# Kernel tuning notes

Measured on AMD Instinct MI355X. Metric: run time of the kernel, lower is better.

Reference implementation:

```python
import jax, jax.numpy as jnp
import numpy as np

N_NODES = 50000
N_EDGES = 800000
C_IN = 128
C_OUT = 128


def setup_inputs() -> dict:
    key = jax.random.key(0)
    k1, k2, k3 = jax.random.split(key, 3)
    x = jax.random.normal(k1, (N_NODES, C_IN), dtype=jnp.float32)
    edge_index = jax.random.randint(k2, (2, N_EDGES), 0, N_NODES, dtype=jnp.int64)
    # Glorot-style init for the GCN weight, zero bias (PyG defaults)
    scale = jnp.sqrt(2.0 / (C_IN + C_OUT)).astype(jnp.float32)
    weight = jax.random.normal(k3, (C_IN, C_OUT), dtype=jnp.float32) * scale
    bias = jnp.zeros((C_OUT,), dtype=jnp.float32)
    return {"x": x, "edge_index": edge_index, "weight": weight, "bias": bias}


def reference(x, edge_index, weight, bias):
    # GCNConv (edge_weight=None): out = D^-1/2 (A+I) D^-1/2 (x @ W) + b, then ReLU.
    # Dropout is identity in eval mode.
    n = x.shape[0]
    loops = jnp.arange(n, dtype=edge_index.dtype)
    src = jnp.concatenate([edge_index[0], loops])  # [E+N] message sources j
    dst = jnp.concatenate([edge_index[1], loops])  # [E+N] aggregation targets i
    ew = jnp.ones(src.shape[0], dtype=x.dtype)
    # degree computed at target nodes (PyG gcn_norm uses col)
    deg = jax.ops.segment_sum(ew, dst, num_segments=n)
    deg_inv_sqrt = jnp.where(deg > 0, jax.lax.rsqrt(jnp.maximum(deg, 1.0)), 0.0)
    norm = deg_inv_sqrt[src] * deg_inv_sqrt[dst]  # [E+N]
    h = x @ weight                                 # [N, C_out]
    msg = h[src] * norm[:, None]                   # gather + scale  [E+N, C_out]
    agg = jax.ops.segment_sum(msg, dst, num_segments=n)  # scatter-add SpMM
    return jax.nn.relu(agg + bias)
```

## Files before the change

### kernel.cpp

```cpp
#include <hip/hip_runtime.h>
#include <cstdint>
#include <cstddef>

#define NCH 128
#define GEMM_ROWS 64
#define XPAD 136
#define CAP 64

typedef short bf16x8 __attribute__((ext_vector_type(8)));
typedef float f32x4 __attribute__((ext_vector_type(4)));
typedef int i32x4 __attribute__((ext_vector_type(4)));

__device__ __forceinline__ int detect_is64(const unsigned int* __restrict__ ei) {
  unsigned int v = ei[((threadIdx.x & 63) << 1) + 1];
  return (__ballot(v != 0u) == 0ULL) ? 1 : 0;
}

__device__ __forceinline__ unsigned short f2bf(float x) {
  unsigned int u = __float_as_uint(x);
  u += 0x7fffu + ((u >> 16) & 1u);
  return (unsigned short)(u >> 16);
}

__device__ __forceinline__ int ei_at(const void* ei, long long i, int is64) {
  return is64 ? (int)((const long long*)ei)[i] : ((const int*)ei)[i];
}

__global__ __launch_bounds__(256) void k_gemm_fill(
    const float* __restrict__ x, const float* __restrict__ W,
    unsigned short* __restrict__ g, int N, const void* __restrict__ ei, int E,
    int* __restrict__ cnt, int* __restrict__ bucket, int gbl) {
  if ((int)blockIdx.x >= gbl) {
    int is64 = detect_is64((const unsigned int*)ei);
    int base = ((int)blockIdx.x - gbl) * 2048 + (int)threadIdx.x * 8;
    if (base >= E) return;
    if (base + 8 <= E) {
      int s[8], d[8];
      if (is64) {
        const long long* ps = (const long long*)ei + base;
        const long long* pd = (const long long*)ei + E + base;
#pragma unroll
        for (int j = 0; j < 8; ++j) { s[j] = (int)ps[j]; d[j] = (int)pd[j]; }
      } else {
        const int4* ps = (const int4*)((const int*)ei + base);
        const int4* pd = (const int4*)((const int*)ei + E + base);
        int4 a = ps[0], b = ps[1], c = pd[0], dd = pd[1];
        s[0] = a.x; s[1] = a.y; s[2] = a.z; s[3] = a.w;
        s[4] = b.x; s[5] = b.y; s[6] = b.z; s[7] = b.w;
        d[0] = c.x; d[1] = c.y; d[2] = c.z; d[3] = c.w;
        d[4] = dd.x; d[5] = dd.y; d[6] = dd.z; d[7] = dd.w;
      }
      int slot[8];
#pragma unroll
      for (int j = 0; j < 8; ++j) slot[j] = atomicAdd(&cnt[d[j]], 1);
#pragma unroll
      for (int j = 0; j < 8; ++j)
        if (slot[j] < CAP) bucket[(size_t)d[j] * CAP + slot[j]] = s[j];
    } else {
      for (int j = 0; j < 8; ++j)
        if (base + j < E) {
          int s = ei_at(ei, base + j, is64);
          int d = ei_at(ei, (long long)E + base + j, is64);
          int slot = atomicAdd(&cnt[d], 1);
          if (slot < CAP) bucket[(size_t)d * CAP + slot] = s;
        }
    }
    return;
  }
  __shared__ unsigned short xbf[GEMM_ROWS * XPAD];
  int t = threadIdx.x;
  int row0 = blockIdx.x * GEMM_ROWS;
#pragma unroll
  for (int j = 0; j < 8; ++j) {
    int idx = t + 256 * j;
    int r = idx >> 5, ch = idx & 31;
    int row = row0 + r;
    float4 v = (row < N) ? ((const float4*)(x + (size_t)row * NCH))[ch]
                         : make_float4(0.f, 0.f, 0.f, 0.f);
    ushort4 p;
    p.x = f2bf(v.x); p.y = f2bf(v.y); p.z = f2bf(v.z); p.w = f2bf(v.w);
    *(ushort4*)&xbf[r * XPAD + ch * 4] = p;
  }
  int lane = t & 63, wv = t >> 6;
  int n0 = wv * 32, l15 = lane & 15, q = lane >> 4;
  bf16x8 B[4][2];
#pragma unroll
  for (int ks = 0; ks < 4; ++ks)
#pragma unroll
    for (int nt = 0; nt < 2; ++nt) {
      int n = n0 + nt * 16 + l15;
      bf16x8 b;
#pragma unroll
      for (int j = 0; j < 8; ++j)
        b[j] = (short)f2bf(W[(size_t)(ks * 32 + q * 8 + j) * NCH + n]);
      B[ks][nt] = b;
    }
  __syncthreads();
  f32x4 acc[4][2];
#pragma unroll
  for (int mt = 0; mt < 4; ++mt)
#pragma unroll
    for (int nt = 0; nt < 2; ++nt)
#pragma unroll
      for (int i = 0; i < 4; ++i) acc[mt][nt][i] = 0.f;
#pragma unroll
  for (int ks = 0; ks < 4; ++ks) {
#pragma unroll
    for (int mt = 0; mt < 4; ++mt) {
      bf16x8 a = *(const bf16x8*)&xbf[(mt * 16 + l15) * XPAD + ks * 32 + q * 8];
      acc[mt][0] = __builtin_amdgcn_mfma_f32_16x16x32_bf16(a, B[ks][0], acc[mt][0], 0, 0, 0);
      acc[mt][1] = __builtin_amdgcn_mfma_f32_16x16x32_bf16(a, B[ks][1], acc[mt][1], 0, 0, 0);
    }
  }
#pragma unroll
  for (int mt = 0; mt < 4; ++mt) {
#pragma unroll
    for (int reg = 0; reg < 4; ++reg) {
      int rl = mt * 16 + q * 4 + reg;
      int row = row0 + rl;
      if (row < N) {
        size_t base = (size_t)row * NCH + n0;
        g[base + l15]      = f2bf(acc[mt][0][reg]);
        g[base + 16 + l15] = f2bf(acc[mt][1][reg]);
      }
    }
  }
}

__device__ __forceinline__ void acc8(float* a, uint4 v, float w) {
  a[0] = fmaf(__uint_as_float(v.x << 16), w, a[0]);
  a[1] = fmaf(__uint_as_float(v.x & 0xffff0000u), w, a[1]);
  a[2] = fmaf(__uint_as_float(v.y << 16), w, a[2]);
  a[3] = fmaf(__uint_as_float(v.y & 0xffff0000u), w, a[3]);
  a[4] = fmaf(__uint_as_float(v.z << 16), w, a[4]);
  a[5] = fmaf(__uint_as_float(v.z & 0xffff0000u), w, a[5]);
  a[6] = fmaf(__uint_as_float(v.w << 16), w, a[6]);
  a[7] = fmaf(__uint_as_float(v.w & 0xffff0000u), w, a[7]);
}

__global__ __launch_bounds__(256) void k_agg(const unsigned short* __restrict__ g,
                                             const int* __restrict__ cnt,
                                             const int* __restrict__ bucket,
                                             const float* __restrict__ bias,
                                             float* __restrict__ out, int N) {
  int i = blockIdx.x * 4 + (threadIdx.x >> 6);
  if (i >= N) return;
  int lane = threadIdx.x & 63;
  int grp = lane >> 4, sl = lane & 15;
  float a[8];
#pragma unroll
  for (int k = 0; k < 8; ++k) a[k] = 0.f;
  int mt = cnt[i];
  float di = rsqrtf((float)(mt + 1));
  int m = mt < CAP ? mt : CAP;
  if (grp == 0) {
    uint4 v = *(const uint4*)(g + (size_t)i * NCH + sl * 8);
    acc8(a, v, di);
  }
  const int* brow = bucket + (size_t)i * CAP;
  int e = 0;
  for (; e + 16 <= m; e += 16) {
    i32x4 sv = *(const i32x4*)(brow + e + 4 * grp);
    float w[4];
    uint4 v[4];
#pragma unroll
    for (int j = 0; j < 4; ++j) {
      v[j] = *(const uint4*)(g + (size_t)sv[j] * NCH + sl * 8);
      w[j] = rsqrtf((float)(cnt[sv[j]] + 1));
    }
#pragma unroll
    for (int j = 0; j < 4; ++j) acc8(a, v[j], w[j]);
  }
  for (; e < m; e += 4) {
    int idx = e + grp;
    int cl = idx < m ? idx : m - 1;
    int s = brow[cl];
    float w = (idx < m) ? rsqrtf((float)(cnt[s] + 1)) : 0.f;
    uint4 v = *(const uint4*)(g + (size_t)s * NCH + sl * 8);
    acc8(a, v, w);
  }
#pragma unroll
  for (int k = 0; k < 8; ++k) {
    a[k] += __shfl_xor(a[k], 16);
    a[k] += __shfl_xor(a[k], 32);
  }
  if (grp == 0) {
    const float4* bb = (const float4*)bias;
    float4 b0 = bb[sl * 2], b1 = bb[sl * 2 + 1];
    f32x4 o0, o1;
    o0[0] = fmaxf(fmaf(a[0], di, b0.x), 0.f);
    o0[1] = fmaxf(fmaf(a[1], di, b0.y), 0.f);
    o0[2] = fmaxf(fmaf(a[2], di, b0.z), 0.f);
    o0[3] = fmaxf(fmaf(a[3], di, b0.w), 0.f);
    o1[0] = fmaxf(fmaf(a[4], di, b1.x), 0.f);
    o1[1] = fmaxf(fmaf(a[5], di, b1.y), 0.f);
    o1[2] = fmaxf(fmaf(a[6], di, b1.z), 0.f);
    o1[3] = fmaxf(fmaf(a[7], di, b1.w), 0.f);
    float* op = out + (size_t)i * NCH + sl * 8;
    __builtin_nontemporal_store(o0, (f32x4*)op);
    __builtin_nontemporal_store(o1, (f32x4*)(op + 4));
  }
}

extern "C" void kernel_launch(void* const* d_in, const int* in_sizes, int n_in,
                              void* d_out, int out_size, void* d_ws, size_t ws_size,
                              hipStream_t stream) {
  const float* x    = (const float*)d_in[0];
  const void*  ei   = d_in[1];
  const float* W    = (const float*)d_in[2];
  const float* bias = (const float*)d_in[3];
  float* out = (float*)d_out;

  int N = out_size / NCH;
  int E = in_sizes[1] / 2;

  char* ws = (char*)d_ws;
  size_t off = 0;
  auto alloc = [&](size_t bytes) -> char* {
    char* p = ws + off;
    off = (off + bytes + 255) & ~(size_t)255;
    return p;
  };
  char* zbase = ws;
  int*            cnt    = (int*)alloc((size_t)N * 4);
  size_t zbytes = off;
  int*            bucket = (int*)alloc((size_t)N * CAP * 4);
  unsigned short* g      = (unsigned short*)alloc((size_t)N * NCH * 2);
  (void)ws_size;

  int gbl  = (N + GEMM_ROWS - 1) / GEMM_ROWS;
  int cbl8 = (E + 2047) / 2048;

  (void)hipMemsetAsync(zbase, 0, zbytes, stream);
  k_gemm_fill<<<gbl + cbl8, 256, 0, stream>>>(x, W, g, N, ei, E, cnt, bucket, gbl);
  k_agg<<<(N + 3) / 4, 256, 0, stream>>>(g, cnt, bucket, bias, out, N);
}
```

Before: 161.9 us.

## Reorder fill blocks first, shrink edges per thread, batch 8 gathers in aggregation

The fused kernel now places the edge-bucketing blocks before the GEMM blocks, so the atomic-heavy fill work is dispatched first. Each fill thread now handles 4 edges instead of 8, which doubles the number of fill blocks. In the aggregation kernel, each 16-lane group now loads 8 neighbor indices and issues 8 row gathers per iteration, covering 32 edges per pass with masked tails. This gives more gathers in flight and removes the separate remainder loop, at the cost of more registers and wasted masked loads for low-degree nodes.

```diff
diff --git a/kernel.cpp b/kernel.cpp
--- a/kernel.cpp
+++ b/kernel.cpp
@@ -9,7 +9,6 @@
 
 typedef short bf16x8 __attribute__((ext_vector_type(8)));
 typedef float f32x4 __attribute__((ext_vector_type(4)));
-typedef int i32x4 __attribute__((ext_vector_type(4)));
 
 __device__ __forceinline__ int detect_is64(const unsigned int* __restrict__ ei) {
   unsigned int v = ei[((threadIdx.x & 63) << 1) + 1];
@@ -26,38 +25,35 @@
   return is64 ? (int)((const long long*)ei)[i] : ((const int*)ei)[i];
 }
 
-__global__ __launch_bounds__(256) void k_gemm_fill(
+__global__ __launch_bounds__(256) void k_fill_gemm(
     const float* __restrict__ x, const float* __restrict__ W,
     unsigned short* __restrict__ g, int N, const void* __restrict__ ei, int E,
-    int* __restrict__ cnt, int* __restrict__ bucket, int gbl) {
-  if ((int)blockIdx.x >= gbl) {
+    int* __restrict__ cnt, int* __restrict__ bucket, int fbl) {
+  if ((int)blockIdx.x < fbl) {
     int is64 = detect_is64((const unsigned int*)ei);
-    int base = ((int)blockIdx.x - gbl) * 2048 + (int)threadIdx.x * 8;
+    int base = (int)blockIdx.x * 1024 + (int)threadIdx.x * 4;
     if (base >= E) return;
-    if (base + 8 <= E) {
-      int s[8], d[8];
+    if (base + 4 <= E) {
+      int s[4], d[4];
       if (is64) {
         const long long* ps = (const long long*)ei + base;
         const long long* pd = (const long long*)ei + E + base;
 #pragma unroll
-        for (int j = 0; j < 8; ++j) { s[j] = (int)ps[j]; d[j] = (int)pd[j]; }
+        for (int j = 0; j < 4; ++j) { s[j] = (int)ps[j]; d[j] = (int)pd[j]; }
       } else {
-        const int4* ps = (const int4*)((const int*)ei + base);
-        const int4* pd = (const int4*)((const int*)ei + E + base);
-        int4 a = ps[0], b = ps[1], c = pd[0], dd = pd[1];
+        int4 a = *(const int4*)((const int*)ei + base);
+        int4 c = *(const int4*)((const int*)ei + E + base);
         s[0] = a.x; s[1] = a.y; s[2] = a.z; s[3] = a.w;
-        s[4] = b.x; s[5] = b.y; s[6] = b.z; s[7] = b.w;
         d[0] = c.x; d[1] = c.y; d[2] = c.z; d[3] = c.w;
-        d[4] = dd.x; d[5] = dd.y; d[6] = dd.z; d[7] = dd.w;
       }
-      int slot[8];
-#pragma unroll
-      for (int j = 0; j < 8; ++j) slot[j] = atomicAdd(&cnt[d[j]], 1);
-#pragma unroll
-      for (int j = 0; j < 8; ++j)
+      int slot[4];
+#pragma unroll
+      for (int j = 0; j < 4; ++j) slot[j] = atomicAdd(&cnt[d[j]], 1);
+#pragma unroll
+      for (int j = 0; j < 4; ++j)
         if (slot[j] < CAP) bucket[(size_t)d[j] * CAP + slot[j]] = s[j];
     } else {
-      for (int j = 0; j < 8; ++j)
+      for (int j = 0; j < 4; ++j)
         if (base + j < E) {
           int s = ei_at(ei, base + j, is64);
           int d = ei_at(ei, (long long)E + base + j, is64);
@@ -69,7 +65,7 @@
   }
   __shared__ unsigned short xbf[GEMM_ROWS * XPAD];
   int t = threadIdx.x;
-  int row0 = blockIdx.x * GEMM_ROWS;
+  int row0 = ((int)blockIdx.x - fbl) * GEMM_ROWS;
 #pragma unroll
   for (int j = 0; j < 8; ++j) {
     int idx = t + 256 * j;
@@ -150,34 +146,32 @@
   float a[8];
 #pragma unroll
   for (int k = 0; k < 8; ++k) a[k] = 0.f;
-  int mt = cnt[i];
-  float di = rsqrtf((float)(mt + 1));
-  int m = mt < CAP ? mt : CAP;
+  int deg = cnt[i];
+  float di = rsqrtf((float)(deg + 1));
+  int m = deg < CAP ? deg : CAP;
   if (grp == 0) {
     uint4 v = *(const uint4*)(g + (size_t)i * NCH + sl * 8);
     acc8(a, v, di);
   }
   const int* brow = bucket + (size_t)i * CAP;
-  int e = 0;
-  for (; e + 16 <= m; e += 16) {
-    i32x4 sv = *(const i32x4*)(brow + e + 4 * grp);
-    float w[4];
-    uint4 v[4];
-#pragma unroll
-    for (int j = 0; j < 4; ++j) {
-      v[j] = *(const uint4*)(g + (size_t)sv[j] * NCH + sl * 8);
-      w[j] = rsqrtf((float)(cnt[sv[j]] + 1));
-    }
-#pragma unroll
-    for (int j = 0; j < 4; ++j) acc8(a, v[j], w[j]);
-  }
-  for (; e < m; e += 4) {
-    int idx = e + grp;
-    int cl = idx < m ? idx : m - 1;
-    int s = brow[cl];
-    float w = (idx < m) ? rsqrtf((float)(cnt[s] + 1)) : 0.f;
-    uint4 v = *(const uint4*)(g + (size_t)s * NCH + sl * 8);
-    acc8(a, v, w);
+  for (int e0 = 0; e0 < m; e0 += 32) {
+    int b = e0 + 8 * grp;
+    int s[8];
+    float w[8];
+#pragma unroll
+    for (int j = 0; j < 8; ++j) {
+      int idx = b + j;
+      int cl = idx < m ? idx : m - 1;
+      s[j] = brow[cl];
+    }
+    uint4 v[8];
+#pragma unroll
+    for (int j = 0; j < 8; ++j) {
+      v[j] = *(const uint4*)(g + (size_t)s[j] * NCH + sl * 8);
+      w[j] = (b + j < m) ? rsqrtf((float)(cnt[s[j]] + 1)) : 0.f;
+    }
+#pragma unroll
+    for (int j = 0; j < 8; ++j) acc8(a, v[j], w[j]);
   }
 #pragma unroll
   for (int k = 0; k < 8; ++k) {
@@ -228,10 +222,10 @@
   unsigned short* g      = (unsigned short*)alloc((size_t)N * NCH * 2);
   (void)ws_size;
 
-  int gbl  = (N + GEMM_ROWS - 1) / GEMM_ROWS;
-  int cbl8 = (E + 2047) / 2048;
+  int gbl = (N + GEMM_ROWS - 1) / GEMM_ROWS;
+  int fbl = (E + 1023) / 1024;
 
   (void)hipMemsetAsync(zbase, 0, zbytes, stream);
-  k_gemm_fill<<<gbl + cbl8, 256, 0, stream>>>(x, W, g, N, ei, E, cnt, bucket, gbl);
+  k_fill_gemm<<<fbl + gbl, 256, 0, stream>>>(x, W, g, N, ei, E, cnt, bucket, fbl);
   k_agg<<<(N + 3) / 4, 256, 0, stream>>>(g, cnt, bucket, bias, out, N);
 }
```

New measurement: 199.1 us. +23.0%, slower.
